# Performance work log

Measured on AMD Instinct MI355X. Metric: run time of the kernel, lower is better.

Reference implementation:

```python
import jax, jax.numpy as jnp
import numpy as np

B, T, C = 2, 1024, 2048
HEAD = 64              # args.head_size_a
H = C // HEAD          # n_head = 32
D_DECAY, D_AAA, D_MV, D_GATE = 96, 96, 64, 256
GN_EPS = 0.00064
EPS_NORM = 1e-12

ARGS = ['x', 'v0', 'xx_r', 'xx_w', 'xx_k', 'xx_v', 'xx_a', 'xx_g',
        'ww_b', 'ww_w1', 'ww_w2', 'aa_b', 'aa_w1', 'aa_w2',
        'vv_b', 'vv_w1', 'vv_w2', 'gg_w1', 'gg_w2',
        'kk_s', 'ka_s', 'rk_s', 'W_r', 'W_k', 'W_v', 'W_o', 'gn_w', 'gn_b']


def setup_inputs() -> dict:
    key = jax.random.key(0)
    it = iter(jax.random.split(key, 32))
    nrm = lambda shape, s=1.0: jax.random.normal(next(it), shape, jnp.float32) * s
    d = {'x': nrm((B, T, C)), 'v0': nrm((B, T, C))}
    for nm in ('xx_r', 'xx_w', 'xx_k', 'xx_v', 'xx_a', 'xx_g',
               'ww_b', 'aa_b', 'vv_b', 'kk_s', 'ka_s'):
        d[nm] = nrm((1, 1, C), 0.5)
    d['ww_w1'] = nrm((C, D_DECAY), 0.02); d['ww_w2'] = nrm((D_DECAY, C), 0.02)
    d['aa_w1'] = nrm((C, D_AAA), 0.02);   d['aa_w2'] = nrm((D_AAA, C), 0.02)
    d['vv_w1'] = nrm((C, D_MV), 0.02);    d['vv_w2'] = nrm((D_MV, C), 0.02)
    d['gg_w1'] = nrm((C, D_GATE), 0.02);  d['gg_w2'] = nrm((D_GATE, C), 0.02)
    d['rk_s'] = nrm((H, HEAD), 0.5)
    d['W_r'] = nrm((C, C), 0.02); d['W_k'] = nrm((C, C), 0.02)
    d['W_v'] = nrm((C, C), 0.02); d['W_o'] = nrm((C, C), 0.02)
    d['gn_w'] = jnp.ones((C,), jnp.float32)
    d['gn_b'] = jnp.zeros((C,), jnp.float32)
    return d


def _rwkv7_op(r, w, k, v, a, b):
    # RWKV7 state recurrence: state[b,h,i,j] (i = value dim, j = key dim),
    # vectorized over (B,H,N), scanned over T.
    to_tbhn = lambda t: t.reshape(B, T, H, HEAD).astype(jnp.float32).transpose(1, 0, 2, 3)
    rT, kT, vT, aT, bT = map(to_tbhn, (r, k, v, a, b))
    wT = jnp.exp(-jnp.exp(to_tbhn(w)))   # decay in (0, 1)
    state0 = jnp.zeros((B, H, HEAD, HEAD), jnp.float32)

    def step(state, inp):
        wt, kt, vt, at, bt, rt = inp     # each [B,H,N]
        sa = jnp.einsum('bhij,bhj->bhi', state, at)
        state = (state * wt[:, :, None, :]
                 + sa[..., None] * bt[:, :, None, :]
                 + vt[..., None] * kt[:, :, None, :])
        return state, jnp.einsum('bhij,bhj->bhi', state, rt)

    _, outs = jax.lax.scan(step, state0, (wT, kT, vT, aT, bT, rT))  # [T,B,H,N]
    return outs.transpose(1, 0, 2, 3).reshape(B, T, C)


def _group_norm(y, gn_w, gn_b):
    # GroupNorm(H, C, eps=0.00064) applied on (B*T, C): per-(token, head) stats over N
    yh = y.reshape(B, T, H, HEAD)
    mu = yh.mean(-1, keepdims=True)
    var = yh.var(-1, keepdims=True)
    yh = (yh - mu) * jax.lax.rsqrt(var + GN_EPS)
    yh = yh * gn_w.reshape(1, 1, H, HEAD) + gn_b.reshape(1, 1, H, HEAD)
    return yh.reshape(B, T, C)


def _forward(x, v0, xx_r, xx_w, xx_k, xx_v, xx_a, xx_g,
             ww_b, ww_w1, ww_w2, aa_b, aa_w1, aa_w2,
             vv_b, vv_w1, vv_w2, gg_w1, gg_w2,
             kk_s, ka_s, rk_s, W_r, W_k, W_v, W_o, gn_w, gn_b):
    # time_shift(x) - x : shift sequence right by one with zero pad
    xx = jnp.pad(x, ((0, 0), (1, 0), (0, 0)))[:, :T, :] - x
    xr = x + xx * xx_r; xw = x + xx * xx_w; xk = x + xx * xx_k
    xv = x + xx * xx_v; xa = x + xx * xx_a; xg = x + xx * xx_g

    r = xr @ W_r
    w = -jax.nn.softplus(-(ww_b + jnp.tanh(xw @ ww_w1) @ ww_w2)) - 0.5  # clamp to (-inf,-0.5)
    k = xk @ W_k
    v = xv @ W_v
    # layer_id > 0: mix with layer-0 value residual
    v = v + (v0 - v) * jax.nn.sigmoid(vv_b + (xv @ vv_w1) @ vv_w2)
    a = jax.nn.sigmoid(aa_b + (xa @ aa_w1) @ aa_w2)
    g = jax.nn.sigmoid(xg @ gg_w1) @ gg_w2

    kk = k * kk_s
    kkh = kk.reshape(B, T, H, HEAD)
    kk = (kkh / jnp.maximum(jnp.linalg.norm(kkh, axis=-1, keepdims=True), EPS_NORM)).reshape(B, T, C)
    k = k * (1.0 + (a - 1.0) * ka_s)

    y = _rwkv7_op(r, w, k, v, -kk, kk * a)
    y = _group_norm(y, gn_w, gn_b)
    # per-head bonus: (r*k*rk_s).sum(-1) * v
    bonus = ((r.reshape(B, T, H, HEAD) * k.reshape(B, T, H, HEAD) * rk_s).sum(-1, keepdims=True)
             * v.reshape(B, T, H, HEAD)).reshape(B, T, C)
    y = y + bonus
    return (y * g) @ W_o


def reference(x, v0, xx_r, xx_w, xx_k, xx_v, xx_a, xx_g,
              ww_b, ww_w1, ww_w2, aa_b, aa_w1, aa_w2,
              vv_b, vv_w1, vv_w2, gg_w1, gg_w2,
              kk_s, ka_s, rk_s, W_r, W_k, W_v, W_o, gn_w, gn_b):
    out = _forward(x, v0, xx_r, xx_w, xx_k, xx_v, xx_a, xx_g,
                   ww_b, ww_w1, ww_w2, aa_b, aa_w1, aa_w2,
                   vv_b, vv_w1, vv_w2, gg_w1, gg_w2,
                   kk_s, ka_s, rk_s, W_r, W_k, W_v, W_o, gn_w, gn_b)
    # layer_id > 0 passes v0 through unchanged
    return (out, v0)
```

## Files before the change

kernel.cpp:

```cpp
#include <hip/hip_runtime.h>
#include <hip/hip_bf16.h>
#include <math.h>

typedef unsigned short u16;
typedef __attribute__((ext_vector_type(4))) unsigned short us4;
typedef __attribute__((ext_vector_type(8))) unsigned short us8;
typedef __attribute__((ext_vector_type(8))) short s8v;
typedef __attribute__((ext_vector_type(4))) float f4v;

#define BB 2
#define TT 1024
#define CC 2048
#define HH 32
#define BT (BB*TT)


__device__ __forceinline__ float bf2f(u16 u) {
  return __uint_as_float(((unsigned int)u) << 16);
}
__device__ __forceinline__ u16 f2bf(float f) {
  unsigned int x = __float_as_uint(f);
  x += 0x7fffu + ((x >> 16) & 1u);
  return (u16)(x >> 16);
}

__global__ __launch_bounds__(256)
void mix_k(const float* __restrict__ x, const float* __restrict__ s,
           u16* __restrict__ out) {
  int idx = blockIdx.x * 256 + threadIdx.x;
  int c = idx & (CC - 1);
  int t = (idx >> 11) & (TT - 1);
  float xv = x[idx];
  float xp = (t == 0) ? 0.f : x[idx - CC];
  out[idx] = f2bf(xv + (xp - xv) * s[c]);
}

__global__ __launch_bounds__(256)
void wt_k(const float* __restrict__ W, u16* __restrict__ Wt, int K, int N) {
  __shared__ u16 tile[32][36];
  const int k0 = blockIdx.x * 32, n0 = blockIdx.y * 32;
  const int tid = threadIdx.x;
  const int r = tid >> 3, c4 = (tid & 7) << 2;
  float4 v = *(const float4*)(W + (size_t)(k0 + r) * N + n0 + c4);
  tile[r][c4 + 0] = f2bf(v.x); tile[r][c4 + 1] = f2bf(v.y);
  tile[r][c4 + 2] = f2bf(v.z); tile[r][c4 + 3] = f2bf(v.w);
  __syncthreads();
  ushort4 o;
  o.x = tile[c4 + 0][r]; o.y = tile[c4 + 1][r];
  o.z = tile[c4 + 2][r]; o.w = tile[c4 + 3][r];
  *(ushort4*)(Wt + (size_t)(n0 + r) * K + k0 + c4) = o;
}

enum { EPI_BF = 0, EPI_F32 = 1, EPI_BIAS_SP = 2, EPI_BIAS_SIG = 3,
       EPI_VMIX = 4 };

template<int EPI>
__global__ __launch_bounds__(256)
void mgemm_k(const u16* __restrict__ A, const u16* __restrict__ Bt,
             float* __restrict__ outF, u16* __restrict__ outB,
             int M, int N, int K,
             const float* __restrict__ bias, const u16* __restrict__ p1,
             const float* __restrict__ p2)
{
  __shared__ alignas(16) u16 As[128][40];
  __shared__ alignas(16) u16 Bs[128][40];
  const int m0 = blockIdx.x * 128;
  const int n0 = blockIdx.y * 128;
  const int tid = threadIdx.x;
  const int lane = tid & 63;
  const int wid = tid >> 6;
  const int wr = wid >> 1, wc = wid & 1;
  const int srow = tid >> 1;
  const int scol = (tid & 1) << 4;
  f4v acc[4][4];
  #pragma unroll
  for (int i = 0; i < 4; ++i)
    #pragma unroll
    for (int j = 0; j < 4; ++j) acc[i][j] = f4v{0.f, 0.f, 0.f, 0.f};

  const int l15 = lane & 15;
  const int lk = (lane >> 4) << 3;
  const int nkt = K >> 5;
  for (int kt = 0; kt < nkt; ++kt) {
    const int k0 = kt << 5;
    const u16* ap = A  + (size_t)(m0 + srow) * K + k0 + scol;
    const u16* bp = Bt + (size_t)(n0 + srow) * K + k0 + scol;
    us8 a0 = *(const us8*)(ap);
    us8 a1 = *(const us8*)(ap + 8);
    us8 b0 = *(const us8*)(bp);
    us8 b1 = *(const us8*)(bp + 8);
    __syncthreads();
    *(us8*)&As[srow][scol]     = a0;
    *(us8*)&As[srow][scol + 8] = a1;
    *(us8*)&Bs[srow][scol]     = b0;
    *(us8*)&Bs[srow][scol + 8] = b1;
    __syncthreads();
    s8v af[4], bfr[4];
    #pragma unroll
    for (int i = 0; i < 4; ++i)
      af[i] = *(const s8v*)&As[wr * 64 + i * 16 + l15][lk];
    #pragma unroll
    for (int j = 0; j < 4; ++j)
      bfr[j] = *(const s8v*)&Bs[wc * 64 + j * 16 + l15][lk];
    #pragma unroll
    for (int i = 0; i < 4; ++i)
      #pragma unroll
      for (int j = 0; j < 4; ++j)
        acc[i][j] = __builtin_amdgcn_mfma_f32_16x16x32_bf16(af[i], bfr[j],
                                                            acc[i][j], 0, 0, 0);
  }
  const int rbase = m0 + wr * 64 + ((lane >> 4) << 2);
  const int cbase = n0 + wc * 64 + l15;
  #pragma unroll
  for (int i = 0; i < 4; ++i) {
    #pragma unroll
    for (int j = 0; j < 4; ++j) {
      f4v c = acc[i][j];
      const int col = cbase + j * 16;
      #pragma unroll
      for (int q = 0; q < 4; ++q) {
        const int row = rbase + i * 16 + q;
        const size_t idx = (size_t)row * N + col;
        const float r = c[q];
        if (EPI == EPI_BF) {
          outB[idx] = f2bf(r);
        } else if (EPI == EPI_F32) {
          outF[idx] = r;
        } else if (EPI == EPI_BIAS_SP) {
          float u = bias[col] + r;
          float z = -u;
          float sp = fmaxf(z, 0.f) + log1pf(expf(-fabsf(z)));
          outB[idx] = f2bf(-sp - 0.5f);
        } else if (EPI == EPI_BIAS_SIG) {
          float u = bias[col] + r;
          outB[idx] = f2bf(1.f / (1.f + expf(-u)));
        } else if (EPI == EPI_VMIX) {
          float u = bias[col] + r;
          float sg = 1.f / (1.f + expf(-u));
          float v = bf2f(p1[idx]);
          float v0v = p2[idx];
          outB[idx] = f2bf(v + (v0v - v) * sg);
        }
      }
    }
  }
}

__global__ __launch_bounds__(256)
void gemm_part_k(const u16* __restrict__ A, const float* __restrict__ W,
                 float* __restrict__ outF, int M, int N, int K, int kchunk,
                 int NP)
{
  __shared__ alignas(16) float As[16][68];
  __shared__ alignas(16) float Bs[16][68];
  const int m0 = blockIdx.x * 64;
  const int n0 = blockIdx.y * 64;
  const int kz = blockIdx.z;
  const int k0base = kz * kchunk;
  const int tid = threadIdx.x;
  const int tx = tid & 15, ty = tid >> 4;
  float acc[4][4] = {{0.f}};
  const int a_m = tid >> 2;
  const int a_k = (tid & 3) << 2;
  const int b_k = tid >> 4;
  const int b_n = (tid & 15) << 2;
  const int niters = kchunk >> 4;
  for (int it = 0; it < niters; ++it) {
    const int k0 = k0base + (it << 4);
    float4 av;
    {
      ushort4 u = *(const ushort4*)(A + (size_t)(m0 + a_m) * K + (k0 + a_k));
      av = make_float4(bf2f(u.x), bf2f(u.y), bf2f(u.z), bf2f(u.w));
    }
    float4 bv;
    {
      int gn = n0 + b_n;
      const float* wp = W + (size_t)(k0 + b_k) * N + gn;
      if (gn + 3 < N) {
        bv = *(const float4*)wp;
      } else {
        bv.x = (gn + 0 < N) ? wp[0] : 0.f;
        bv.y = (gn + 1 < N) ? wp[1] : 0.f;
        bv.z = (gn + 2 < N) ? wp[2] : 0.f;
        bv.w = (gn + 3 < N) ? wp[3] : 0.f;
      }
    }
    __syncthreads();
    As[a_k + 0][a_m] = av.x; As[a_k + 1][a_m] = av.y;
    As[a_k + 2][a_m] = av.z; As[a_k + 3][a_m] = av.w;
    Bs[b_k][b_n + 0] = bv.x; Bs[b_k][b_n + 1] = bv.y;
    Bs[b_k][b_n + 2] = bv.z; Bs[b_k][b_n + 3] = bv.w;
    __syncthreads();
    #pragma unroll
    for (int kk = 0; kk < 16; ++kk) {
      float4 a4 = *(const float4*)&As[kk][ty << 2];
      float4 b4 = *(const float4*)&Bs[kk][tx << 2];
      float ar[4] = {a4.x, a4.y, a4.z, a4.w};
      float br[4] = {b4.x, b4.y, b4.z, b4.w};
      #pragma unroll
      for (int i = 0; i < 4; ++i)
        #pragma unroll
        for (int j = 0; j < 4; ++j)
          acc[i][j] = fmaf(ar[i], br[j], acc[i][j]);
    }
  }
  #pragma unroll
  for (int i = 0; i < 4; ++i) {
    int gm = m0 + (ty << 2) + i;
    #pragma unroll
    for (int j = 0; j < 4; ++j) {
      int gn = n0 + (tx << 2) + j;
      if (gn >= N) continue;
      outF[((size_t)kz * M + gm) * NP + gn] = acc[i][j];
    }
  }
}

__global__ __launch_bounds__(256)
void reduce_k(const float* __restrict__ part, u16* __restrict__ out,
              int M, int D, int NP, int nz, int act)
{
  int idx = blockIdx.x * 256 + threadIdx.x;
  if (idx >= M * D) return;
  int t = idx / D, n = idx - t * D;
  float s = 0.f;
  for (int z = 0; z < nz; ++z) s += part[((size_t)z * M + t) * NP + n];
  if (act == 1) s = tanhf(s);
  else if (act == 2) s = 1.f / (1.f + expf(-s));
  out[idx] = f2bf(s);
}

__global__ __launch_bounds__(256)
void prep_k(const u16* __restrict__ k_in, const u16* __restrict__ a_in,
            const u16* __restrict__ r_in, const u16* __restrict__ w_in,
            const float* __restrict__ kk_s, const float* __restrict__ ka_s,
            u16* __restrict__ ao_out, u16* __restrict__ bo_out,
            u16* __restrict__ k_out, u16* __restrict__ wd_out,
            u16* __restrict__ rw_out, float2* __restrict__ scal)
{
  int tid = threadIdx.x;
  int lane = tid & 63;
  int wv = tid >> 6;
  int hidx = blockIdx.x * 4 + wv;
  int h = hidx & (HH - 1);
  int c = (h << 6) + lane;
  size_t base = ((size_t)hidx << 6) + lane;
  float k = bf2f(k_in[base]);
  float kk = k * kk_s[c];
  float ss = kk * kk;
  for (int off = 32; off; off >>= 1) ss += __shfl_xor(ss, off, 64);
  float kkn = kk / fmaxf(sqrtf(ss), 1e-12f);
  float a = bf2f(a_in[base]);
  float r = bf2f(r_in[base]);
  float kf = k * (1.f + (a - 1.f) * ka_s[c]);
  float wd = expf(-expf(bf2f(w_in[base])));
  float bo = kkn * a;
  ao_out[base] = f2bf(-kkn);
  bo_out[base] = f2bf(bo);
  k_out[base]  = f2bf(kf);
  wd_out[base] = f2bf(wd);
  rw_out[base] = f2bf(wd * r);
  float kr = kf * r, br = bo * r;
  kr += __shfl_xor(kr, 1, 64);  br += __shfl_xor(br, 1, 64);
  kr += __shfl_xor(kr, 2, 64);  br += __shfl_xor(br, 2, 64);
  kr += __shfl_xor(kr, 4, 64);  br += __shfl_xor(br, 4, 64);
  kr += __shfl_xor(kr, 8, 64);  br += __shfl_xor(br, 8, 64);
  kr += __shfl_xor(kr, 16, 64); br += __shfl_xor(br, 16, 64);
  kr += __shfl_xor(kr, 32, 64); br += __shfl_xor(br, 32, 64);
  if (lane == 0) scal[hidx] = make_float2(kr, br);
}

__global__ __launch_bounds__(256)
void prep2_k(u16* __restrict__ wd, u16* __restrict__ ao,
             u16* __restrict__ bo, u16* __restrict__ rw,
             const u16* __restrict__ kf, float4* __restrict__ scal4)
{
  int tid = threadIdx.x;
  int lane = tid & 63;
  int wv = tid >> 6;
  int hpidx = blockIdx.x * 4 + wv;
  int h = hpidx & (HH - 1);
  int btp = hpidx >> 5;
  int tp = btp & (TT / 2 - 1);
  int b = btp >> 9;
  size_t be = ((size_t)(b * TT + 2 * tp)) * CC + (h << 6) + lane;
  size_t bodd = be + CC;
  float wd1 = bf2f(wd[be]),  wd2 = bf2f(wd[bodd]);
  float ao2 = bf2f(ao[bodd]), rw2 = bf2f(rw[bodd]);
  float bo1 = bf2f(bo[be]),  k1  = bf2f(kf[be]);
  float cba = bo1 * ao2, ckb = k1 * ao2, crb = bo1 * rw2, crk = k1 * rw2;
  #pragma unroll
  for (int off = 32; off; off >>= 1) {
    cba += __shfl_xor(cba, off, 64);
    ckb += __shfl_xor(ckb, off, 64);
    crb += __shfl_xor(crb, off, 64);
    crk += __shfl_xor(crk, off, 64);
  }
  wd[be]   = f2bf(wd1 * wd2);
  wd[bodd] = f2bf(k1 * wd2);
  ao[bodd] = f2bf(wd1 * ao2);
  bo[be]   = f2bf(bo1 * wd2);
  rw[bodd] = f2bf(wd1 * rw2);
  if (lane == 0) scal4[hpidx] = make_float4(cba, ckb, crb, crk);
}

__global__ __launch_bounds__(256)
void rec_k(const u16* __restrict__ rw, const u16* __restrict__ wd,
           const u16* __restrict__ kv, const u16* __restrict__ v,
           const u16* __restrict__ ao, const u16* __restrict__ bo,
           const float2* __restrict__ scal, const float4* __restrict__ scal4,
           u16* __restrict__ y)
{
  const int gw = blockIdx.x * 4 + (threadIdx.x >> 6);
  const int lane = threadIdx.x & 63;
  const int sub = lane & 15;
  const int grp = lane >> 4;
  const int bh = gw >> 4;
  const int rblk = gw & 15;
  const int i = rblk * 4 + grp;
  const int b = bh >> 5, h = bh & (HH - 1);
  const size_t base0 = ((size_t)b * TT) * CC + (h << 6);
  const size_t vecb = base0 + (sub << 2);
  const size_t vb   = base0 + i;
  const int sbase = b * TT * HH + h;
  const int pbase = b * (TT / 2) * HH + h;
  float s0 = 0.f, s1 = 0.f, s2 = 0.f, s3 = 0.f;

  us4 W12, KW1, AO1, WA2, BW1, BO2, RW1, WR2, K2;
  float V1, V2; float2 SE, SO; float4 S4;
#define PLOAD(TP) do {                                                  \
    const size_t be_ = vecb + (size_t)(2 * (TP)) * CC;                  \
    const size_t bo_ = be_ + CC;                                        \
    W12 = *(const us4*)(wd + be_);  KW1 = *(const us4*)(wd + bo_);      \
    AO1 = *(const us4*)(ao + be_);  WA2 = *(const us4*)(ao + bo_);      \
    BW1 = *(const us4*)(bo + be_);  BO2 = *(const us4*)(bo + bo_);      \
    RW1 = *(const us4*)(rw + be_);  WR2 = *(const us4*)(rw + bo_);      \
    K2  = *(const us4*)(kv + bo_);                                      \
    V1 = bf2f(v[vb + (size_t)(2 * (TP)) * CC]);                         \
    V2 = bf2f(v[vb + (size_t)(2 * (TP) + 1) * CC]);                     \
    SE = scal[sbase + (2 * (TP)) * HH];                                 \
    SO = scal[sbase + (2 * (TP) + 1) * HH];                             \
    S4 = scal4[pbase + (TP) * HH];                                      \
  } while (0)

  PLOAD(0);
  for (int tp = 0; tp < TT / 2; ++tp) {
    const float w0 = bf2f(W12[0]), w1 = bf2f(W12[1]),
                w2 = bf2f(W12[2]), w3 = bf2f(W12[3]);
    const float kw0 = bf2f(KW1[0]), kw1_ = bf2f(KW1[1]),
                kw2 = bf2f(KW1[2]), kw3 = bf2f(KW1[3]);
    const float a0 = bf2f(AO1[0]), a1 = bf2f(AO1[1]),
                a2 = bf2f(AO1[2]), a3 = bf2f(AO1[3]);
    const float x0 = bf2f(WA2[0]), x1 = bf2f(WA2[1]),
                x2 = bf2f(WA2[2]), x3 = bf2f(WA2[3]);
    const float bw0 = bf2f(BW1[0]), bw1_ = bf2f(BW1[1]),
                bw2 = bf2f(BW1[2]), bw3 = bf2f(BW1[3]);
    const float b0 = bf2f(BO2[0]), b1 = bf2f(BO2[1]),
                b2 = bf2f(BO2[2]), b3 = bf2f(BO2[3]);
    const float e0 = bf2f(RW1[0]), e1 = bf2f(RW1[1]),
                e2 = bf2f(RW1[2]), e3 = bf2f(RW1[3]);
    const float f0 = bf2f(WR2[0]), f1 = bf2f(WR2[1]),
                f2 = bf2f(WR2[2]), f3 = bf2f(WR2[3]);
    const float k0 = bf2f(K2[0]), k1 = bf2f(K2[1]),
                k2 = bf2f(K2[2]), k3 = bf2f(K2[3]);
    const float v1c = V1, v2c = V2;
    const float kr1 = SE.x, br1 = SE.y, kr2 = SO.x, br2 = SO.y;
    const float cba = S4.x, ckb = S4.y, crb = S4.z, crk = S4.w;
    if (tp + 1 < TT / 2) PLOAD(tp + 1);
    float u1 = fmaf(s3, a3, fmaf(s2, a2, fmaf(s1, a1, s0 * a0)));
    float u2 = fmaf(s3, x3, fmaf(s2, x2, fmaf(s1, x1, s0 * x0)));
    float q1 = fmaf(s3, e3, fmaf(s2, e2, fmaf(s1, e1, s0 * e0)));
    float q2 = fmaf(s3, f3, fmaf(s2, f2, fmaf(s1, f1, s0 * f0)));
    u1 += __shfl_xor(u1, 1, 64);  u2 += __shfl_xor(u2, 1, 64);
    q1 += __shfl_xor(q1, 1, 64);  q2 += __shfl_xor(q2, 1, 64);
    u1 += __shfl_xor(u1, 2, 64);  u2 += __shfl_xor(u2, 2, 64);
    q1 += __shfl_xor(q1, 2, 64);  q2 += __shfl_xor(q2, 2, 64);
    u1 += __shfl_xor(u1, 4, 64);  u2 += __shfl_xor(u2, 4, 64);
    q1 += __shfl_xor(q1, 4, 64);  q2 += __shfl_xor(q2, 4, 64);
    u1 += __shfl_xor(u1, 8, 64);  u2 += __shfl_xor(u2, 8, 64);
    q1 += __shfl_xor(q1, 8, 64);  q2 += __shfl_xor(q2, 8, 64);
    const float sac = fmaf(ckb, v1c, fmaf(cba, u1, u2));
    const float y1 = fmaf(br1, u1, fmaf(kr1, v1c, q1));
    const float y2 = fmaf(br2, sac, fmaf(kr2, v2c,
                       fmaf(crb, u1, fmaf(crk, v1c, q2))));
    s0 = fmaf(v2c, k0, fmaf(v1c, kw0, fmaf(sac, b0, fmaf(u1, bw0, s0 * w0))));
    s1 = fmaf(v2c, k1, fmaf(v1c, kw1_, fmaf(sac, b1, fmaf(u1, bw1_, s1 * w1))));
    s2 = fmaf(v2c, k2, fmaf(v1c, kw2, fmaf(sac, b2, fmaf(u1, bw2, s2 * w2))));
    s3 = fmaf(v2c, k3, fmaf(v1c, kw3, fmaf(sac, b3, fmaf(u1, bw3, s3 * w3))));
    if (sub == 0) {
      y[vb + (size_t)(2 * tp) * CC] = f2bf(y1);
      y[vb + (size_t)(2 * tp + 1) * CC] = f2bf(y2);
    }
  }
#undef PLOAD
}

__global__ __launch_bounds__(256)
void gn_k(u16* __restrict__ y, const u16* __restrict__ r,
          const u16* __restrict__ k, const u16* __restrict__ v,
          const u16* __restrict__ g, const float* __restrict__ rk_s,
          const float* __restrict__ gn_w, const float* __restrict__ gn_b)
{
  int tid = threadIdx.x, lane = tid & 63, wv = tid >> 6;
  int hidx = blockIdx.x * 4 + wv;
  int h = hidx & (HH - 1);
  int c = (h << 6) + lane;
  size_t base = ((size_t)hidx << 6) + lane;
  float yv = bf2f(y[base]), rv = bf2f(r[base]), kv = bf2f(k[base]);
  float vv = bf2f(v[base]), gv = bf2f(g[base]);
  float bsum = rv * kv * rk_s[c];
  float s1 = yv, s2 = yv * yv;
  for (int off = 32; off; off >>= 1) {
    s1 += __shfl_xor(s1, off, 64);
    s2 += __shfl_xor(s2, off, 64);
    bsum += __shfl_xor(bsum, off, 64);
  }
  float mu = s1 * (1.f / 64.f);
  float var = s2 * (1.f / 64.f) - mu * mu;
  float rstd = rsqrtf(var + 0.00064f);
  float z = (yv - mu) * rstd * gn_w[c] + gn_b[c];
  y[base] = f2bf((z + bsum * vv) * gv);
}

__global__ __launch_bounds__(256)
void copy_v0(const float* __restrict__ v0, float* __restrict__ out) {
  int idx = blockIdx.x * 256 + threadIdx.x;
  ((float4*)out)[idx] = ((const float4*)v0)[idx];
}

__global__ __launch_bounds__(256)
void zero_out(float* __restrict__ out) {
  int idx = blockIdx.x * 256 + threadIdx.x;
  ((float4*)out)[idx] = make_float4(0.f, 0.f, 0.f, 0.f);
}

extern "C" void kernel_launch(void* const* d_in, const int* in_sizes, int n_in,
                              void* d_out, int out_size, void* d_ws, size_t ws_size,
                              hipStream_t stream) {
  (void)n_in; (void)out_size;
  const bool dictOrder = (in_sizes[9] == CC);
  int IX[28];
  if (dictOrder) {
    const int m[28] = {0,1,2,3,4,5,6,7, 8,13,14, 9,15,16, 10,17,18, 19,20,
                       11,12,21, 22,23,24,25, 26,27};
    for (int i = 0; i < 28; ++i) IX[i] = m[i];
  } else {
    for (int i = 0; i < 28; ++i) IX[i] = i;
  }
  const float* x     = (const float*)d_in[IX[0]];
  const float* v0    = (const float*)d_in[IX[1]];
  const float* xx_r  = (const float*)d_in[IX[2]];
  const float* xx_w  = (const float*)d_in[IX[3]];
  const float* xx_k  = (const float*)d_in[IX[4]];
  const float* xx_v  = (const float*)d_in[IX[5]];
  const float* xx_a  = (const float*)d_in[IX[6]];
  const float* xx_g  = (const float*)d_in[IX[7]];
  const float* ww_b  = (const float*)d_in[IX[8]];
  const float* ww_w1 = (const float*)d_in[IX[9]];
  const float* ww_w2 = (const float*)d_in[IX[10]];
  const float* aa_b  = (const float*)d_in[IX[11]];
  const float* aa_w1 = (const float*)d_in[IX[12]];
  const float* aa_w2 = (const float*)d_in[IX[13]];
  const float* vv_b  = (const float*)d_in[IX[14]];
  const float* vv_w1 = (const float*)d_in[IX[15]];
  const float* vv_w2 = (const float*)d_in[IX[16]];
  const float* gg_w1 = (const float*)d_in[IX[17]];
  const float* gg_w2 = (const float*)d_in[IX[18]];
  const float* kk_s  = (const float*)d_in[IX[19]];
  const float* ka_s  = (const float*)d_in[IX[20]];
  const float* rk_s  = (const float*)d_in[IX[21]];
  const float* W_r   = (const float*)d_in[IX[22]];
  const float* W_k   = (const float*)d_in[IX[23]];
  const float* W_v   = (const float*)d_in[IX[24]];
  const float* W_o   = (const float*)d_in[IX[25]];
  const float* gn_w  = (const float*)d_in[IX[26]];
  const float* gn_b  = (const float*)d_in[IX[27]];

  const size_t NBTC = (size_t)BT * CC;
  dim3 blk(256);
  const int grid4f = (int)(NBTC / 4 / 256);

  const size_t WS_NEED = 7 * NBTC * sizeof(u16);
  float* outF = (float*)d_out;
  if (ws_size < WS_NEED || d_ws == nullptr) {
    zero_out<<<grid4f, blk, 0, stream>>>(outF);
    copy_v0<<<grid4f, blk, 0, stream>>>(v0, outF + NBTC);
    return;
  }

  u16* W16   = (u16*)d_ws;
  u16* R0 = W16 + 0 * NBTC;
  u16* R1 = W16 + 1 * NBTC;
  u16* R2 = W16 + 2 * NBTC;
  u16* R3 = W16 + 3 * NBTC;
  u16* R4 = W16 + 4 * NBTC;
  u16* R5 = W16 + 5 * NBTC;
  u16* R6 = W16 + 6 * NBTC;
  float* partY = (float*)R3;
  float* partG = (float*)R5;
  u16* ws_y = (u16*)(outF + NBTC);
  float2* scal = (float2*)(ws_y + NBTC);
  float4* scal4 = (float4*)(ws_y + NBTC + (size_t)BT * HH * 4);

  const int gridMix = (BT * CC) / 256;
  dim3 gM(BT / 128, 2048 / 128);

  mix_k<<<gridMix, blk, 0, stream>>>(x, xx_w, R6);
  gemm_part_k<<<dim3(32, 2, 8), blk, 0, stream>>>(R6, ww_w1, partY,
      BT, 96, 2048, 256, 128);
  reduce_k<<<(BT * 96 + 255) / 256, blk, 0, stream>>>(partY, R0, BT, 96, 128, 8, 1);
  wt_k<<<dim3(3, 64), blk, 0, stream>>>(ww_w2, R1, 96, 2048);
  mgemm_k<EPI_BIAS_SP><<<gM, blk, 0, stream>>>(R0, R1, nullptr, R5,
      BT, 2048, 96, ww_b, nullptr, nullptr);

  mix_k<<<gridMix, blk, 0, stream>>>(x, xx_a, R6);
  gemm_part_k<<<dim3(32, 2, 8), blk, 0, stream>>>(R6, aa_w1, partY,
      BT, 96, 2048, 256, 128);
  reduce_k<<<(BT * 96 + 255) / 256, blk, 0, stream>>>(partY, R0, BT, 96, 128, 8, 0);
  wt_k<<<dim3(3, 64), blk, 0, stream>>>(aa_w2, R1, 96, 2048);
  mgemm_k<EPI_BIAS_SIG><<<gM, blk, 0, stream>>>(R0, R1, nullptr, R4,
      BT, 2048, 96, aa_b, nullptr, nullptr);

  mix_k<<<gridMix, blk, 0, stream>>>(x, xx_v, R6);
  wt_k<<<dim3(64, 64), blk, 0, stream>>>(W_v, R1, 2048, 2048);
  mgemm_k<EPI_BF><<<gM, blk, 0, stream>>>(R6, R1, nullptr, R2,
      BT, 2048, 2048, nullptr, nullptr, nullptr);
  gemm_part_k<<<dim3(32, 1, 8), blk, 0, stream>>>(R6, vv_w1, partY,
      BT, 64, 2048, 256, 64);
  reduce_k<<<(BT * 64 + 255) / 256, blk, 0, stream>>>(partY, R0, BT, 64, 64, 8, 0);
  wt_k<<<dim3(2, 64), blk, 0, stream>>>(vv_w2, R1, 64, 2048);
  mgemm_k<EPI_VMIX><<<gM, blk, 0, stream>>>(R0, R1, nullptr, R2,
      BT, 2048, 64, vv_b, R2, v0);

  mix_k<<<gridMix, blk, 0, stream>>>(x, xx_k, R6);
  wt_k<<<dim3(64, 64), blk, 0, stream>>>(W_k, R3, 2048, 2048);
  mgemm_k<EPI_BF><<<gM, blk, 0, stream>>>(R6, R3, nullptr, R1,
      BT, 2048, 2048, nullptr, nullptr, nullptr);

  mix_k<<<gridMix, blk, 0, stream>>>(x, xx_r, R6);
  wt_k<<<dim3(64, 64), blk, 0, stream>>>(W_r, R3, 2048, 2048);
  mgemm_k<EPI_BF><<<gM, blk, 0, stream>>>(R6, R3, nullptr, R0,
      BT, 2048, 2048, nullptr, nullptr, nullptr);

  prep_k<<<BT * HH / 4, blk, 0, stream>>>(R1, R4, R0, R5, kk_s, ka_s,
                                          R3, R4, R1, R5, R6, scal);

  prep2_k<<<BT / 2 * HH / 4, blk, 0, stream>>>(R5, R3, R4, R6, R1, scal4);

  rec_k<<<256, blk, 0, stream>>>(R6, R5, R1, R2, R3, R4, scal, scal4, ws_y);

  mix_k<<<gridMix, blk, 0, stream>>>(x, xx_g, R6);
  gemm_part_k<<<dim3(32, 4, 2), blk, 0, stream>>>(R6, gg_w1, partG,
      BT, 256, 2048, 1024, 256);
  reduce_k<<<(BT * 256 + 255) / 256, blk, 0, stream>>>(partG, R3, BT, 256, 256, 2, 2);
  wt_k<<<dim3(8, 64), blk, 0, stream>>>(gg_w2, R5, 256, 2048);
  mgemm_k<EPI_BF><<<gM, blk, 0, stream>>>(R3, R5, nullptr, R4,
      BT, 2048, 256, nullptr, nullptr, nullptr);

  gn_k<<<BT * HH / 4, blk, 0, stream>>>(ws_y, R0, R1, R2, R4,
                                        rk_s, gn_w, gn_b);

  wt_k<<<dim3(64, 64), blk, 0, stream>>>(W_o, R5, 2048, 2048);
  mgemm_k<EPI_F32><<<gM, blk, 0, stream>>>(ws_y, R5, outF, nullptr,
      BT, 2048, 2048, nullptr, nullptr, nullptr);

  copy_v0<<<grid4f, blk, 0, stream>>>(v0, outF + NBTC);
}
```

Measured before the change: 866.3 us.

## Load GEMM tiles straight into LDS with XOR swizzle and 64-wide K steps

The MFMA GEMM now uses global_load_lds to copy tiles directly from global memory into shared memory, skipping the register staging step. The shared-memory layout becomes unpadded 64-wide rows with an XOR swizzle to avoid bank conflicts, and each K step doubles to 64, halving the number of barriers. Because K must now be a multiple of 64, the rank-96 low-rank path is padded to 128: reduce_k writes zeros in the extra columns and wt_k and mgemm_k gain leading-dimension arguments. The padded tail of the transposed weight buffer is never written, so it relies on the zero activations cancelling whatever stale data sits there.

Measured after the change: 809.3 us. 6.6% less time.

```diff
diff --git a/kernel.cpp b/kernel.cpp
--- a/kernel.cpp
+++ b/kernel.cpp
@@ -22,6 +22,12 @@
   unsigned int x = __float_as_uint(f);
   x += 0x7fffu + ((x >> 16) & 1u);
   return (u16)(x >> 16);
+}
+
+__device__ __forceinline__ void gload16(const u16* g, u16* l) {
+  __builtin_amdgcn_global_load_lds(
+      (const __attribute__((address_space(1))) void*)g,
+      (__attribute__((address_space(3))) void*)l, 16, 0, 0);
 }
 
 __global__ __launch_bounds__(256)
@@ -36,7 +42,8 @@
 }
 
 __global__ __launch_bounds__(256)
-void wt_k(const float* __restrict__ W, u16* __restrict__ Wt, int K, int N) {
+void wt_k(const float* __restrict__ W, u16* __restrict__ Wt, int K, int N,
+          int Kp) {
   __shared__ u16 tile[32][36];
   const int k0 = blockIdx.x * 32, n0 = blockIdx.y * 32;
   const int tid = threadIdx.x;
@@ -48,7 +55,7 @@
   ushort4 o;
   o.x = tile[c4 + 0][r]; o.y = tile[c4 + 1][r];
   o.z = tile[c4 + 2][r]; o.w = tile[c4 + 3][r];
-  *(ushort4*)(Wt + (size_t)(n0 + r) * K + k0 + c4) = o;
+  *(ushort4*)(Wt + (size_t)(n0 + r) * Kp + k0 + c4) = o;
 }
 
 enum { EPI_BF = 0, EPI_F32 = 1, EPI_BIAS_SP = 2, EPI_BIAS_SIG = 3,
@@ -58,20 +65,18 @@
 __global__ __launch_bounds__(256)
 void mgemm_k(const u16* __restrict__ A, const u16* __restrict__ Bt,
              float* __restrict__ outF, u16* __restrict__ outB,
-             int M, int N, int K,
+             int M, int N, int K, int lda, int ldb,
              const float* __restrict__ bias, const u16* __restrict__ p1,
              const float* __restrict__ p2)
 {
-  __shared__ alignas(16) u16 As[128][40];
-  __shared__ alignas(16) u16 Bs[128][40];
+  __shared__ alignas(16) u16 As[128 * 64];
+  __shared__ alignas(16) u16 Bs[128 * 64];
   const int m0 = blockIdx.x * 128;
   const int n0 = blockIdx.y * 128;
   const int tid = threadIdx.x;
   const int lane = tid & 63;
   const int wid = tid >> 6;
   const int wr = wid >> 1, wc = wid & 1;
-  const int srow = tid >> 1;
-  const int scol = (tid & 1) << 4;
   f4v acc[4][4];
   #pragma unroll
   for (int i = 0; i < 4; ++i)
@@ -79,37 +84,47 @@
     for (int j = 0; j < 4; ++j) acc[i][j] = f4v{0.f, 0.f, 0.f, 0.f};
 
   const int l15 = lane & 15;
-  const int lk = (lane >> 4) << 3;
-  const int nkt = K >> 5;
+  const int lq = lane >> 4;
+  const int nkt = K >> 6;
   for (int kt = 0; kt < nkt; ++kt) {
-    const int k0 = kt << 5;
-    const u16* ap = A  + (size_t)(m0 + srow) * K + k0 + scol;
-    const u16* bp = Bt + (size_t)(n0 + srow) * K + k0 + scol;
-    us8 a0 = *(const us8*)(ap);
-    us8 a1 = *(const us8*)(ap + 8);
-    us8 b0 = *(const us8*)(bp);
-    us8 b1 = *(const us8*)(bp + 8);
+    const int k0 = kt << 6;
     __syncthreads();
-    *(us8*)&As[srow][scol]     = a0;
-    *(us8*)&As[srow][scol + 8] = a1;
-    *(us8*)&Bs[srow][scol]     = b0;
-    *(us8*)&Bs[srow][scol + 8] = b1;
+    #pragma unroll
+    for (int a = 0; a < 4; ++a) {
+      const int blkU = (wid * 4 + a) * 64;
+      const int U = blkU + lane;
+      const int row = U >> 3;
+      const int u = U & 7;
+      const int col = ((u ^ (row & 7)) << 3);
+      gload16(A  + (size_t)(m0 + row) * lda + k0 + col, &As[blkU * 8]);
+      gload16(Bt + (size_t)(n0 + row) * ldb + k0 + col, &Bs[blkU * 8]);
+    }
     __syncthreads();
-    s8v af[4], bfr[4];
     #pragma unroll
-    for (int i = 0; i < 4; ++i)
-      af[i] = *(const s8v*)&As[wr * 64 + i * 16 + l15][lk];
-    #pragma unroll
-    for (int j = 0; j < 4; ++j)
-      bfr[j] = *(const s8v*)&Bs[wc * 64 + j * 16 + l15][lk];
-    #pragma unroll
-    for (int i = 0; i < 4; ++i)
+    for (int h = 0; h < 2; ++h) {
+      s8v af[4], bfr[4];
       #pragma unroll
-      for (int j = 0; j < 4; ++j)
-        acc[i][j] = __builtin_amdgcn_mfma_f32_16x16x32_bf16(af[i], bfr[j],
-                                                            acc[i][j], 0, 0, 0);
-  }
-  const int rbase = m0 + wr * 64 + ((lane >> 4) << 2);
+      for (int i = 0; i < 4; ++i) {
+        const int row = wr * 64 + i * 16 + l15;
+        const int u = (h * 4 + lq) ^ (row & 7);
+        af[i] = *(const s8v*)&As[row * 64 + u * 8];
+      }
+      #pragma unroll
+      for (int j = 0; j < 4; ++j) {
+        const int row = wc * 64 + j * 16 + l15;
+        const int u = (h * 4 + lq) ^ (row & 7);
+        bfr[j] = *(const s8v*)&Bs[row * 64 + u * 8];
+      }
+      #pragma unroll
+      for (int i = 0; i < 4; ++i)
+        #pragma unroll
+        for (int j = 0; j < 4; ++j)
+          acc[i][j] = __builtin_amdgcn_mfma_f32_16x16x32_bf16(af[i], bfr[j],
+                                                              acc[i][j],
+                                                              0, 0, 0);
+    }
+  }
+  const int rbase = m0 + wr * 64 + (lq << 2);
   const int cbase = n0 + wc * 64 + l15;
   #pragma unroll
   for (int i = 0; i < 4; ++i) {
@@ -218,15 +233,17 @@
 
 __global__ __launch_bounds__(256)
 void reduce_k(const float* __restrict__ part, u16* __restrict__ out,
-              int M, int D, int NP, int nz, int act)
+              int M, int D, int NP, int nz, int act, int Dp)
 {
   int idx = blockIdx.x * 256 + threadIdx.x;
-  if (idx >= M * D) return;
-  int t = idx / D, n = idx - t * D;
+  if (idx >= M * Dp) return;
+  int t = idx / Dp, n = idx - t * Dp;
   float s = 0.f;
-  for (int z = 0; z < nz; ++z) s += part[((size_t)z * M + t) * NP + n];
-  if (act == 1) s = tanhf(s);
-  else if (act == 2) s = 1.f / (1.f + expf(-s));
+  if (n < D) {
+    for (int z = 0; z < nz; ++z) s += part[((size_t)z * M + t) * NP + n];
+    if (act == 1) s = tanhf(s);
+    else if (act == 2) s = 1.f / (1.f + expf(-s));
+  }
   out[idx] = f2bf(s);
 }
 
@@ -508,39 +525,39 @@
   mix_k<<<gridMix, blk, 0, stream>>>(x, xx_w, R6);
   gemm_part_k<<<dim3(32, 2, 8), blk, 0, stream>>>(R6, ww_w1, partY,
       BT, 96, 2048, 256, 128);
-  reduce_k<<<(BT * 96 + 255) / 256, blk, 0, stream>>>(partY, R0, BT, 96, 128, 8, 1);
-  wt_k<<<dim3(3, 64), blk, 0, stream>>>(ww_w2, R1, 96, 2048);
+  reduce_k<<<(BT * 128) / 256, blk, 0, stream>>>(partY, R0, BT, 96, 128, 8, 1, 128);
+  wt_k<<<dim3(3, 64), blk, 0, stream>>>(ww_w2, R1, 96, 2048, 128);
   mgemm_k<EPI_BIAS_SP><<<gM, blk, 0, stream>>>(R0, R1, nullptr, R5,
-      BT, 2048, 96, ww_b, nullptr, nullptr);
+      BT, 2048, 128, 128, 128, ww_b, nullptr, nullptr);
 
   mix_k<<<gridMix, blk, 0, stream>>>(x, xx_a, R6);
   gemm_part_k<<<dim3(32, 2, 8), blk, 0, stream>>>(R6, aa_w1, partY,
       BT, 96, 2048, 256, 128);
-  reduce_k<<<(BT * 96 + 255) / 256, blk, 0, stream>>>(partY, R0, BT, 96, 128, 8, 0);
-  wt_k<<<dim3(3, 64), blk, 0, stream>>>(aa_w2, R1, 96, 2048);
+  reduce_k<<<(BT * 128) / 256, blk, 0, stream>>>(partY, R0, BT, 96, 128, 8, 0, 128);
+  wt_k<<<dim3(3, 64), blk, 0, stream>>>(aa_w2, R1, 96, 2048, 128);
   mgemm_k<EPI_BIAS_SIG><<<gM, blk, 0, stream>>>(R0, R1, nullptr, R4,
-      BT, 2048, 96, aa_b, nullptr, nullptr);
+      BT, 2048, 128, 128, 128, aa_b, nullptr, nullptr);
 
   mix_k<<<gridMix, blk, 0, stream>>>(x, xx_v, R6);
-  wt_k<<<dim3(64, 64), blk, 0, stream>>>(W_v, R1, 2048, 2048);
+  wt_k<<<dim3(64, 64), blk, 0, stream>>>(W_v, R1, 2048, 2048, 2048);
   mgemm_k<EPI_BF><<<gM, blk, 0, stream>>>(R6, R1, nullptr, R2,
-      BT, 2048, 2048, nullptr, nullptr, nullptr);
+      BT, 2048, 2048, 2048, 2048, nullptr, nullptr, nullptr);
   gemm_part_k<<<dim3(32, 1, 8), blk, 0, stream>>>(R6, vv_w1, partY,
       BT, 64, 2048, 256, 64);
-  reduce_k<<<(BT * 64 + 255) / 256, blk, 0, stream>>>(partY, R0, BT, 64, 64, 8, 0);
-  wt_k<<<dim3(2, 64), blk, 0, stream>>>(vv_w2, R1, 64, 2048);
+  reduce_k<<<(BT * 64) / 256, blk, 0, stream>>>(partY, R0, BT, 64, 64, 8, 0, 64);
+  wt_k<<<dim3(2, 64), blk, 0, stream>>>(vv_w2, R1, 64, 2048, 64);
   mgemm_k<EPI_VMIX><<<gM, blk, 0, stream>>>(R0, R1, nullptr, R2,
-      BT, 2048, 64, vv_b, R2, v0);
+      BT, 2048, 64, 64, 64, vv_b, R2, v0);
 
   mix_k<<<gridMix, blk, 0, stream>>>(x, xx_k, R6);
-  wt_k<<<dim3(64, 64), blk, 0, stream>>>(W_k, R3, 2048, 2048);
+  wt_k<<<dim3(64, 64), blk, 0, stream>>>(W_k, R3, 2048, 2048, 2048);
   mgemm_k<EPI_BF><<<gM, blk, 0, stream>>>(R6, R3, nullptr, R1,
-      BT, 2048, 2048, nullptr, nullptr, nullptr);
+      BT, 2048, 2048, 2048, 2048, nullptr, nullptr, nullptr);
 
   mix_k<<<gridMix, blk, 0, stream>>>(x, xx_r, R6);
-  wt_k<<<dim3(64, 64), blk, 0, stream>>>(W_r, R3, 2048, 2048);
+  wt_k<<<dim3(64, 64), blk, 0, stream>>>(W_r, R3, 2048, 2048, 2048);
   mgemm_k<EPI_BF><<<gM, blk, 0, stream>>>(R6, R3, nullptr, R0,
-      BT, 2048, 2048, nullptr, nullptr, nullptr);
+      BT, 2048, 2048, 2048, 2048, nullptr, nullptr, nullptr);
 
   prep_k<<<BT * HH / 4, blk, 0, stream>>>(R1, R4, R0, R5, kk_s, ka_s,
                                           R3, R4, R1, R5, R6, scal);
@@ -552,17 +569,17 @@
   mix_k<<<gridMix, blk, 0, stream>>>(x, xx_g, R6);
   gemm_part_k<<<dim3(32, 4, 2), blk, 0, stream>>>(R6, gg_w1, partG,
       BT, 256, 2048, 1024, 256);
-  reduce_k<<<(BT * 256 + 255) / 256, blk, 0, stream>>>(partG, R3, BT, 256, 256, 2, 2);
-  wt_k<<<dim3(8, 64), blk, 0, stream>>>(gg_w2, R5, 256, 2048);
+  reduce_k<<<(BT * 256) / 256, blk, 0, stream>>>(partG, R3, BT, 256, 256, 2, 2, 256);
+  wt_k<<<dim3(8, 64), blk, 0, stream>>>(gg_w2, R5, 256, 2048, 256);
   mgemm_k<EPI_BF><<<gM, blk, 0, stream>>>(R3, R5, nullptr, R4,
-      BT, 2048, 256, nullptr, nullptr, nullptr);
+      BT, 2048, 256, 256, 256, nullptr, nullptr, nullptr);
 
   gn_k<<<BT * HH / 4, blk, 0, stream>>>(ws_y, R0, R1, R2, R4,
                                         rk_s, gn_w, gn_b);
 
-  wt_k<<<dim3(64, 64), blk, 0, stream>>>(W_o, R5, 2048, 2048);
+  wt_k<<<dim3(64, 64), blk, 0, stream>>>(W_o, R5, 2048, 2048, 2048);
   mgemm_k<EPI_F32><<<gM, blk, 0, stream>>>(ws_y, R5, outF, nullptr,
-      BT, 2048, 2048, nullptr, nullptr, nullptr);
+      BT, 2048, 2048, 2048, 2048, nullptr, nullptr, nullptr);
 
   copy_v0<<<grid4f, blk, 0, stream>>>(v0, outF + NBTC);
 }
```
